# Performance work log

Measured on AMD Instinct MI355X. Metric: run time of the kernel, lower is better.

Reference implementation:

```python
import jax, jax.numpy as jnp
import numpy as np

HIDDEN = 1024
NUM_HEAD = 16
HEAD_DIM = HIDDEN // NUM_HEAD


def setup_inputs() -> dict:
    key = jax.random.key(0)
    ks = jax.random.split(key, 9)
    B, S = 1, 4096
    scale = 1.0 / np.sqrt(HIDDEN)
    inp = {
        "x": jax.random.normal(ks[0], (B, S, HIDDEN), dtype=jnp.float32),
        "wq": jax.random.normal(ks[1], (HIDDEN, HIDDEN), dtype=jnp.float32) * scale,
        "bq": jnp.zeros((HIDDEN,), dtype=jnp.float32),
        "wk": jax.random.normal(ks[2], (HIDDEN, HIDDEN), dtype=jnp.float32) * scale,
        "bk": jnp.zeros((HIDDEN,), dtype=jnp.float32),
        "wv": jax.random.normal(ks[3], (HIDDEN, HIDDEN), dtype=jnp.float32) * scale,
        "bv": jnp.zeros((HIDDEN,), dtype=jnp.float32),
        "wo": jax.random.normal(ks[4], (HIDDEN, HIDDEN), dtype=jnp.float32) * scale,
        "bo": jnp.zeros((HIDDEN,), dtype=jnp.float32),
    }
    return inp


def reference(x, wq, bq, wk, bk, wv, bv, wo, bo):
    B, S, _ = x.shape
    # QKV projections (torch Linear: x @ W.T + b)
    def split_heads(t):
        return t.reshape(B, S, NUM_HEAD, HEAD_DIM).transpose(0, 2, 1, 3)  # [B,H,S,D]
    q = split_heads(x @ wq.T + bq)
    k = split_heads(x @ wk.T + bk)
    v = split_heads(x @ wv.T + bv)
    # scaled dot-product scores: [B,H,S,S]
    scores = jnp.einsum('bhsd,bhtd->bhst', q, k) / jnp.sqrt(jnp.float32(HEAD_DIM))
    # faithful double softmax over the key axis (no mask; dropout = eval identity)
    attn = jax.nn.softmax(scores, axis=-1)
    attn = jax.nn.softmax(attn, axis=-1)
    out = jnp.einsum('bhst,bhtd->bhsd', attn, v)  # [B,H,S,D]
    out = out.transpose(0, 2, 1, 3).reshape(B, S, HIDDEN)
    return out @ wo.T + bo
```

## Files before the change

### kernel.cpp

```cpp
#include <hip/hip_runtime.h>
#include <hip/hip_bf16.h>
#include <stdint.h>

#define S 4096
#define HID 1024
#define NH 16
#define DH 64

typedef __attribute__((ext_vector_type(8))) short short8;
typedef __attribute__((ext_vector_type(2))) float f32x2;
typedef __attribute__((ext_vector_type(4))) float f32x4;
typedef __attribute__((ext_vector_type(16))) float f32x16;
typedef __attribute__((ext_vector_type(4))) unsigned int u32x4;

#define VMCNT8 asm volatile("s_waitcnt vmcnt(8)" ::: "memory")
#define VMCNT0 asm volatile("s_waitcnt vmcnt(0)" ::: "memory")
#define LGKM0  asm volatile("s_waitcnt lgkmcnt(0)" ::: "memory")

__device__ __forceinline__ unsigned short f2bf(float f) {
  unsigned int u = __builtin_bit_cast(unsigned int, f);
  u += 0x7FFF + ((u >> 16) & 1);
  return (unsigned short)(u >> 16);
}
__device__ __forceinline__ unsigned int pktrunc(float lo, float hi) {
  return __builtin_amdgcn_perm(__builtin_bit_cast(unsigned int, hi),
                               __builtin_bit_cast(unsigned int, lo), 0x07060302u);
}
__device__ __forceinline__ void gload16(const unsigned short* g, unsigned short* l) {
  __builtin_amdgcn_global_load_lds((const __attribute__((address_space(1))) unsigned int*)g,
                                   (__attribute__((address_space(3))) unsigned int*)l, 16, 0, 0);
}

__global__ __launch_bounds__(256) void cast_kernel(
    const float* __restrict__ x,  const float* __restrict__ wq,
    const float* __restrict__ wk, const float* __restrict__ wv,
    const float* __restrict__ wo,
    unsigned short* __restrict__ xb,  unsigned short* __restrict__ wqb,
    unsigned short* __restrict__ wkb, unsigned short* __restrict__ wvb,
    unsigned short* __restrict__ wob, float* __restrict__ vsum)
{
  int y = blockIdx.y;
  const float* src; unsigned short* dst; int n;
  if      (y == 0) { src = x;  dst = xb;  n = S * HID; }
  else if (y == 1) { src = wq; dst = wqb; n = HID * HID; }
  else if (y == 2) { src = wk; dst = wkb; n = HID * HID; }
  else if (y == 3) { src = wv; dst = wvb; n = HID * HID; }
  else             { src = wo; dst = wob; n = HID * HID; }
  if (y == 0 && blockIdx.x == 0) {
    f32x4 z = {0.f, 0.f, 0.f, 0.f};
    reinterpret_cast<f32x4*>(vsum)[threadIdx.x] = z;
  }
  int i = (blockIdx.x * 256 + threadIdx.x) * 4;
  if (i < n) {
    float4 v = *reinterpret_cast<const float4*>(src + i);
    ushort4 o;
    o.x = f2bf(v.x); o.y = f2bf(v.y); o.z = f2bf(v.z); o.w = f2bf(v.w);
    *reinterpret_cast<ushort4*>(dst + i) = o;
  }
}

__device__ __forceinline__ void gemm128(
    const unsigned short* __restrict__ A, const unsigned short* __restrict__ W,
    unsigned short* As, unsigned short* Bs, f32x4 acc[4][4], int row0, int col0)
{
  const int tid = threadIdx.x;
  const int wave = tid >> 6, lane = tid & 63, quad = lane >> 4, l16 = lane & 15;
  const int wr = (wave >> 1) * 64, wc = (wave & 1) * 64;
  const int srow = lane >> 2, sseg = lane & 3;
  const f32x4 z = {0.f, 0.f, 0.f, 0.f};
  #pragma unroll
  for (int i = 0; i < 4; i++)
    #pragma unroll
    for (int j = 0; j < 4; j++) acc[i][j] = z;

  for (int k0 = 0; k0 < HID; k0 += 32) {
    __syncthreads();
    #pragma unroll
    for (int c = 0; c < 2; c++) {
      const int rbase = c * 64 + wave * 16;
      gload16(A + (size_t)(row0 + rbase + srow) * HID + k0 + sseg * 8, As + rbase * 32);
      gload16(W + (size_t)(col0 + rbase + srow) * HID + k0 + sseg * 8, Bs + rbase * 32);
    }
    __syncthreads();

    short8 af[4], bfr[4];
    #pragma unroll
    for (int i = 0; i < 4; i++)
      af[i] = *reinterpret_cast<const short8*>(As + (wr + i * 16 + l16) * 32 + quad * 8);
    #pragma unroll
    for (int j = 0; j < 4; j++)
      bfr[j] = *reinterpret_cast<const short8*>(Bs + (wc + j * 16 + l16) * 32 + quad * 8);
    #pragma unroll
    for (int i = 0; i < 4; i++)
      #pragma unroll
      for (int j = 0; j < 4; j++)
        acc[i][j] = __builtin_amdgcn_mfma_f32_16x16x32_bf16(af[i], bfr[j], acc[i][j], 0, 0, 0);
  }
}

__global__ __launch_bounds__(256) void qkv_gemm_kernel(
    const unsigned short* __restrict__ X,
    const unsigned short* __restrict__ Wq, const unsigned short* __restrict__ Wk,
    const unsigned short* __restrict__ Wv,
    const float* __restrict__ bq, const float* __restrict__ bk, const float* __restrict__ bv,
    unsigned short* __restrict__ Qo, unsigned short* __restrict__ K2o, unsigned short* __restrict__ Vbo,
    float* __restrict__ Vsum)
{
  __shared__ unsigned short As[128 * 32];
  __shared__ unsigned short Bs[128 * 32];
  __shared__ unsigned short Ep[16384];
  const int zsel = blockIdx.z;
  const unsigned short* W = (zsel == 0) ? Wq : (zsel == 1) ? Wk : Wv;
  const float* bias        = (zsel == 0) ? bq : (zsel == 1) ? bk : bv;
  const int row0 = blockIdx.x * 128, col0 = blockIdx.y * 128;
  f32x4 acc[4][4];
  gemm128(X, W, As, Bs, acc, row0, col0);

  const int tid = threadIdx.x;
  const int wave = tid >> 6, lane = tid & 63, quad = lane >> 4, l16 = lane & 15;
  const int wr = (wave >> 1) * 64, wc = (wave & 1) * 64;
  const int h0 = col0 >> 6, g0 = row0 >> 5;

  if (zsel == 0) {
    const float osc = 0.18033688011112042f;
    #pragma unroll
    for (int j = 0; j < 4; j++) {
      int rc = wc + j * 16 + l16;
      float bb = bias[col0 + rc];
      int hh = rc >> 6, d = rc & 63;
      #pragma unroll
      for (int i = 0; i < 4; i++)
        #pragma unroll
        for (int rr = 0; rr < 4; rr++) {
          int srel = wr + i * 16 + quad * 4 + rr;
          Ep[hh * 8192 + srel * 64 + d] = f2bf((acc[i][j][rr] + bb) * osc);
        }
    }
  } else if (zsel == 1) {
    #pragma unroll
    for (int j = 0; j < 4; j++) {
      int rc = wc + j * 16 + l16;
      float bb = bias[col0 + rc];
      int hh = rc >> 6, dh = rc & 63;
      int c = dh >> 4, hfk = (dh >> 3) & 1, j8 = dh & 7;
      #pragma unroll
      for (int i = 0; i < 4; i++)
        #pragma unroll
        for (int rr = 0; rr < 4; rr++) {
          int srel = wr + i * 16 + quad * 4 + rr;
          int gl = srel >> 5, l32k = srel & 31;
          Ep[(hh * 4 + gl) * 2048 + (c * 64 + hfk * 32 + l32k) * 8 + j8] =
              f2bf(acc[i][j][rr] + bb);
        }
    }
  } else {
    #pragma unroll
    for (int j = 0; j < 4; j++) {
      int rc = wc + j * 16 + l16;
      float bb = bias[col0 + rc];
      int hh = rc >> 6, dh = rc & 63;
      int ng = dh >> 5, l32v = dh & 31;
      int hf_v = quad & 1, jj0 = (quad >> 1) * 4;
      float colsum = 0.f;
      #pragma unroll
      for (int i = 0; i < 4; i++) {
        int gt4 = (wr + i * 16) >> 5;
        int grp = i & 1;
        float v0 = acc[i][j][0] + bb, v1 = acc[i][j][1] + bb;
        float v2 = acc[i][j][2] + bb, v3 = acc[i][j][3] + bb;
        colsum += (v0 + v1) + (v2 + v3);
        ushort4 pv;
        pv.x = f2bf(v0); pv.y = f2bf(v1); pv.z = f2bf(v2); pv.w = f2bf(v3);
        *reinterpret_cast<ushort4*>(
            Ep + (((hh * 4 + gt4) * 2 + grp) * 2 + ng) * 512 + (hf_v * 32 + l32v) * 8 + jj0) = pv;
      }
      colsum += __shfl_xor(colsum, 16);
      colsum += __shfl_xor(colsum, 32);
      if (quad == 0) atomicAdd(&Vsum[col0 + rc], colsum);
    }
  }
  __syncthreads();

  #pragma unroll
  for (int it = 0; it < 8; it++) {
    int flat = it * 2048 + tid * 8;
    u32x4 v = *reinterpret_cast<const u32x4*>(Ep + flat);
    if (zsel == 0) {
      int hh = flat >> 13;
      size_t goff = ((size_t)(h0 + hh) * S + row0) * 64 + (flat & 8191);
      *reinterpret_cast<u32x4*>(Qo + goff) = v;
    } else if (zsel == 1) {
      int sp = flat >> 11, hh = sp >> 2, g4 = sp & 3;
      size_t goff = (size_t)((h0 + hh) * 128 + g0 + g4) * 2048 + (flat & 2047);
      *reinterpret_cast<u32x4*>(K2o + goff) = v;
    } else {
      int sp = flat >> 9;
      int ng = sp & 1, grp = (sp >> 1) & 1, gt4 = (sp >> 2) & 3, hh = sp >> 4;
      size_t goff = (size_t)((((h0 + hh) * 128 + g0 + gt4) * 2 + grp) * 2 + ng) * 512 + (flat & 511);
      *reinterpret_cast<u32x4*>(Vbo + goff) = v;
    }
  }
}

__global__ __launch_bounds__(256) void out_gemm_kernel(
    const unsigned short* __restrict__ A, const unsigned short* __restrict__ W,
    const float* __restrict__ be, float* __restrict__ dst)
{
  __shared__ unsigned short As[128 * 32];
  __shared__ unsigned short Bs[128 * 32];
  const int row0 = blockIdx.x * 128, col0 = blockIdx.y * 128;
  f32x4 acc[4][4];
  gemm128(A, W, As, Bs, acc, row0, col0);

  const int tid = threadIdx.x;
  const int wave = tid >> 6, lane = tid & 63, quad = lane >> 4, l16 = lane & 15;
  const int wr = (wave >> 1) * 64, wc = (wave & 1) * 64;
  #pragma unroll
  for (int j = 0; j < 4; j++) {
    int n = col0 + wc + j * 16 + l16;
    float bb = be[n];
    #pragma unroll
    for (int i = 0; i < 4; i++)
      #pragma unroll
      for (int rr = 0; rr < 4; rr++) {
        int s = row0 + wr + i * 16 + quad * 4 + rr;
        dst[(size_t)s * HID + n] = acc[i][j][rr] + bb;
      }
  }
}

__global__ __launch_bounds__(256) void biasfold_kernel(
    const float* __restrict__ Vsum, const float* __restrict__ wo,
    const float* __restrict__ bo, float* __restrict__ be)
{
  const int n = blockIdx.x * 4 + (threadIdx.x >> 6);
  const int l = threadIdx.x & 63;
  float acc = 0.f;
  #pragma unroll
  for (int i = 0; i < 16; i++)
    acc += Vsum[l + 64 * i] * wo[(size_t)n * HID + l + 64 * i];
  #pragma unroll
  for (int off = 32; off >= 1; off >>= 1) acc += __shfl_xor(acc, off);
  if (l == 0) be[n] = bo[n] + acc * (1.f / 4097.f);
}

struct AttnState {
  short8 qf[2][4];
  f32x16 Oa[2][2];
  f32x16 zacc;
  f32x2  zp[2];
};

__device__ __forceinline__ void loadregs(
    const unsigned short* kb, const unsigned short* vb,
    short8 (&kf)[4], short8 (&vf)[4])
{
  #pragma unroll
  for (int c = 0; c < 4; c++)
    kf[c] = *reinterpret_cast<const short8*>(kb + c * 512);
  #pragma unroll
  for (int w = 0; w < 4; w++)
    vf[w] = *reinterpret_cast<const short8*>(vb + w * 512);
}

__device__ __forceinline__ void attn_compute(
    const short8 (&kf)[4], const short8 (&vfr)[4], AttnState& st)
{
  #pragma unroll
  for (int qh = 0; qh < 2; qh++) {
    f32x16 acc = __builtin_amdgcn_mfma_f32_32x32x16_bf16(kf[0], st.qf[qh][0], st.zacc, 0, 0, 0);
    #pragma unroll
    for (int c = 1; c < 4; c++)
      acc = __builtin_amdgcn_mfma_f32_32x32x16_bf16(kf[c], st.qf[qh][c], acc, 0, 0, 0);

    unsigned int D[8];
    #pragma unroll
    for (int m = 0; m < 8; m++) {
      float t0 = __builtin_amdgcn_exp2f(acc[2 * m]);
      float t1 = __builtin_amdgcn_exp2f(acc[2 * m + 1]);
      f32x2 t = {t0, t1};
      st.zp[qh] += t;
      D[m] = pktrunc(t0, t1);
    }
    u32x4 dv0 = {D[0], D[1], D[2], D[3]};
    u32x4 dv1 = {D[4], D[5], D[6], D[7]};
    short8 A0 = __builtin_bit_cast(short8, dv0);
    short8 A1 = __builtin_bit_cast(short8, dv1);

    st.Oa[qh][0] = __builtin_amdgcn_mfma_f32_32x32x16_bf16(A0, vfr[0], st.Oa[qh][0], 0, 0, 0);
    st.Oa[qh][1] = __builtin_amdgcn_mfma_f32_32x32x16_bf16(A0, vfr[1], st.Oa[qh][1], 0, 0, 0);
    st.Oa[qh][0] = __builtin_amdgcn_mfma_f32_32x32x16_bf16(A1, vfr[2], st.Oa[qh][0], 0, 0, 0);
    st.Oa[qh][1] = __builtin_amdgcn_mfma_f32_32x32x16_bf16(A1, vfr[3], st.Oa[qh][1], 0, 0, 0);
  }
}

__device__ __forceinline__ void stage_tile(
    const unsigned short* gK, const unsigned short* gV,
    unsigned short* lK, unsigned short* lV)
{
  #pragma unroll
  for (int i = 0; i < 4; i++) gload16(gK + i * 512, lK + i * 512);
  #pragma unroll
  for (int i = 0; i < 4; i++) gload16(gV + i * 512, lV + i * 512);
}

__global__ __launch_bounds__(256, 2) void attn_kernel(
    const unsigned short* __restrict__ Q, const unsigned short* __restrict__ K2,
    const unsigned short* __restrict__ Vb, unsigned short* __restrict__ OUT)
{
  __shared__ unsigned short T[4][2][2][2048];
  __shared__ float Zl[256];
  float* Ored = reinterpret_cast<float*>(&T[0][0][0][0]);

  const int lin = blockIdx.y * 64 + blockIdx.x;
  const int xcd = lin & 7, idx = lin >> 3;
  const int h = xcd * 2 + (idx >> 6);
  const int q0 = (idx & 63) * 64;

  const int tid = threadIdx.x;
  const int wave = tid >> 6, lane = tid & 63, hf = lane >> 5, l32 = lane & 31;

  AttnState st;
  #pragma unroll
  for (int qh = 0; qh < 2; qh++) {
    const unsigned short* qrow = Q + (size_t)(h * S + q0 + qh * 32 + l32) * DH;
    #pragma unroll
    for (int c = 0; c < 4; c++)
      st.qf[qh][c] = *reinterpret_cast<const short8*>(qrow + c * 16 + hf * 8);
  }
  #pragma unroll
  for (int r = 0; r < 16; r++) {
    st.zacc[r] = 0.f;
    st.Oa[0][0][r] = 0.f; st.Oa[0][1][r] = 0.f;
    st.Oa[1][0][r] = 0.f; st.Oa[1][1][r] = 0.f;
  }
  st.zp[0] = (f32x2){0.f, 0.f};
  st.zp[1] = (f32x2){0.f, 0.f};

  const unsigned short* Kb  = K2 + (size_t)h * 128 * 2048;
  const unsigned short* Vbb = Vb + (size_t)h * 128 * 2048;

  const unsigned short* gK = Kb  + (size_t)wave * 2048 + (size_t)lane * 8;
  const unsigned short* gV = Vbb + (size_t)wave * 2048 + (size_t)lane * 8;
  unsigned short* lK0 = &T[wave][0][0][0];
  unsigned short* lV0 = &T[wave][0][1][0];
  unsigned short* lK1 = &T[wave][1][0][0];
  unsigned short* lV1 = &T[wave][1][1][0];
  const unsigned short* kb0 = &T[wave][0][0][0] + lane * 8;
  const unsigned short* vb0 = &T[wave][0][1][0] + lane * 8;
  const unsigned short* kb1 = &T[wave][1][0][0] + lane * 8;
  const unsigned short* vb1 = &T[wave][1][1][0] + lane * 8;
  const ptrdiff_t STR = 4 * 2048;

  short8 kA[4], vA[4], kB[4], vB[4];

  stage_tile(gK, gV, lK0, lV0); gK += STR; gV += STR;
  VMCNT0;
  loadregs(kb0, vb0, kA, vA);
  stage_tile(gK, gV, lK1, lV1); gK += STR; gV += STR;
  LGKM0;

  for (int p = 0; p < 15; p++) {
    stage_tile(gK, gV, lK0, lV0); gK += STR; gV += STR;
    VMCNT8;
    loadregs(kb1, vb1, kB, vB);
    attn_compute(kA, vA, st);
    LGKM0;
    stage_tile(gK, gV, lK1, lV1); gK += STR; gV += STR;
    VMCNT8;
    loadregs(kb0, vb0, kA, vA);
    attn_compute(kB, vB, st);
    LGKM0;
  }
  VMCNT0;
  loadregs(kb1, vb1, kB, vB);
  attn_compute(kA, vA, st);
  attn_compute(kB, vB, st);

  __syncthreads();
  {
    float za = st.zp[0][0] + st.zp[0][1];
    float zb = st.zp[1][0] + st.zp[1][1];
    za += __shfl_xor(za, 32);
    zb += __shfl_xor(zb, 32);
    if (hf == 0) {
      Zl[wave * 64 + l32]      = za;
      Zl[wave * 64 + 32 + l32] = zb;
    }
    float* Ow = Ored + wave * 4096;
    #pragma unroll
    for (int qh = 0; qh < 2; qh++)
      #pragma unroll
      for (int ng = 0; ng < 2; ng++)
        #pragma unroll
        for (int r = 0; r < 16; r++) {
          const int row = (r & 3) + 8 * (r >> 2) + 4 * hf;
          Ow[(qh * 32 + row) * 64 + ng * 32 + l32] = st.Oa[qh][ng][r];
        }
  }
  __syncthreads();
  {
    const int q = tid >> 2, d0 = (tid & 3) * 16;
    const float* O0 = Ored + q * 64 + d0;
    f32x4 s0 = *reinterpret_cast<const f32x4*>(O0);
    f32x4 s1 = *reinterpret_cast<const f32x4*>(O0 + 4);
    f32x4 s2 = *reinterpret_cast<const f32x4*>(O0 + 8);
    f32x4 s3 = *reinterpret_cast<const f32x4*>(O0 + 12);
    #pragma unroll
    for (int w = 1; w < 4; w++) {
      const float* Ow = Ored + w * 4096 + q * 64 + d0;
      s0 += *reinterpret_cast<const f32x4*>(Ow);
      s1 += *reinterpret_cast<const f32x4*>(Ow + 4);
      s2 += *reinterpret_cast<const f32x4*>(Ow + 8);
      s3 += *reinterpret_cast<const f32x4*>(Ow + 12);
    }
    const float zt = Zl[q] + Zl[64 + q] + Zl[128 + q] + Zl[192 + q];
    const float rz = 1.f / (zt * 4097.f);
    unsigned short* op = OUT + (size_t)(q0 + q) * HID + h * DH + d0;
    ushort4 u;
    u.x = f2bf(s0[0] * rz); u.y = f2bf(s0[1] * rz);
    u.z = f2bf(s0[2] * rz); u.w = f2bf(s0[3] * rz);
    *reinterpret_cast<ushort4*>(op) = u;
    u.x = f2bf(s1[0] * rz); u.y = f2bf(s1[1] * rz);
    u.z = f2bf(s1[2] * rz); u.w = f2bf(s1[3] * rz);
    *reinterpret_cast<ushort4*>(op + 4) = u;
    u.x = f2bf(s2[0] * rz); u.y = f2bf(s2[1] * rz);
    u.z = f2bf(s2[2] * rz); u.w = f2bf(s2[3] * rz);
    *reinterpret_cast<ushort4*>(op + 8) = u;
    u.x = f2bf(s3[0] * rz); u.y = f2bf(s3[1] * rz);
    u.z = f2bf(s3[2] * rz); u.w = f2bf(s3[3] * rz);
    *reinterpret_cast<ushort4*>(op + 12) = u;
  }
}

extern "C" void kernel_launch(void* const* d_in, const int* in_sizes, int n_in,
                              void* d_out, int out_size, void* d_ws, size_t ws_size,
                              hipStream_t stream) {
  const float* x  = (const float*)d_in[0];
  const float* wq = (const float*)d_in[1];
  const float* bq = (const float*)d_in[2];
  const float* wk = (const float*)d_in[3];
  const float* bk = (const float*)d_in[4];
  const float* wv = (const float*)d_in[5];
  const float* bv = (const float*)d_in[6];
  const float* wo = (const float*)d_in[7];
  const float* bo = (const float*)d_in[8];
  float* out = (float*)d_out;

  char* ws = (char*)d_ws;
  unsigned short* xb  = (unsigned short*)(ws);
  unsigned short* wqb = (unsigned short*)(ws + (8u  << 20));
  unsigned short* wkb = (unsigned short*)(ws + (10u << 20));
  unsigned short* wvb = (unsigned short*)(ws + (12u << 20));
  unsigned short* wob = (unsigned short*)(ws + (14u << 20));
  unsigned short* qw  = (unsigned short*)(ws + (16u << 20));
  unsigned short* k2  = (unsigned short*)(ws + (24u << 20));
  unsigned short* vb  = (unsigned short*)(ws + (32u << 20));
  float* vsum         = (float*)(ws + (40u << 20));
  float* be           = (float*)(ws + (40u << 20) + 65536);
  unsigned short* aw  = xb;

  cast_kernel<<<dim3(4096, 5), 256, 0, stream>>>(x, wq, wk, wv, wo, xb, wqb, wkb, wvb, wob, vsum);
  qkv_gemm_kernel<<<dim3(32, 8, 3), 256, 0, stream>>>(xb, wqb, wkb, wvb, bq, bk, bv, qw, k2, vb, vsum);
  biasfold_kernel<<<dim3(256), 256, 0, stream>>>(vsum, wo, bo, be);
  attn_kernel<<<dim3(64, 16), 256, 0, stream>>>(qw, k2, vb, aw);
  out_gemm_kernel<<<dim3(32, 8, 1), 256, 0, stream>>>(aw, wob, be, out);
}
```

Before: 234.3 us.

## Fold bias-fold kernel into attention launch, compact cast grid, add MFMA priority

The separate biasfold kernel becomes an extra row of blocks (blockIdx.y==16) in the attention launch, which removes one kernel launch and its serialization. The cast kernel's grid is reshaped to 1024x8 with no idle blocks and no bounds check. s_setprio hints are placed around the MFMA sequences in the attention inner loop to favor matrix issue. The extra attention blocks finish quickly but take scheduling slots. Because the bias blocks sit at the end of the grid, the XCD mapping of the attention blocks is unchanged.

```diff
diff --git a/kernel.cpp b/kernel.cpp
--- a/kernel.cpp
+++ b/kernel.cpp
@@ -39,24 +39,22 @@
     unsigned short* __restrict__ wkb, unsigned short* __restrict__ wvb,
     unsigned short* __restrict__ wob, float* __restrict__ vsum)
 {
-  int y = blockIdx.y;
-  const float* src; unsigned short* dst; int n;
-  if      (y == 0) { src = x;  dst = xb;  n = S * HID; }
-  else if (y == 1) { src = wq; dst = wqb; n = HID * HID; }
-  else if (y == 2) { src = wk; dst = wkb; n = HID * HID; }
-  else if (y == 3) { src = wv; dst = wvb; n = HID * HID; }
-  else             { src = wo; dst = wob; n = HID * HID; }
-  if (y == 0 && blockIdx.x == 0) {
+  const int y = blockIdx.y, bx = blockIdx.x;
+  const float* src; unsigned short* dst; int cx;
+  if (y < 4)       { src = x;  dst = xb;  cx = y * 1024 + bx; }
+  else if (y == 4) { src = wq; dst = wqb; cx = bx; }
+  else if (y == 5) { src = wk; dst = wkb; cx = bx; }
+  else if (y == 6) { src = wv; dst = wvb; cx = bx; }
+  else             { src = wo; dst = wob; cx = bx; }
+  if (y == 4 && bx == 0) {
     f32x4 z = {0.f, 0.f, 0.f, 0.f};
     reinterpret_cast<f32x4*>(vsum)[threadIdx.x] = z;
   }
-  int i = (blockIdx.x * 256 + threadIdx.x) * 4;
-  if (i < n) {
-    float4 v = *reinterpret_cast<const float4*>(src + i);
-    ushort4 o;
-    o.x = f2bf(v.x); o.y = f2bf(v.y); o.z = f2bf(v.z); o.w = f2bf(v.w);
-    *reinterpret_cast<ushort4*>(dst + i) = o;
-  }
+  int i = (cx * 256 + threadIdx.x) * 4;
+  float4 v = *reinterpret_cast<const float4*>(src + i);
+  ushort4 o;
+  o.x = f2bf(v.x); o.y = f2bf(v.y); o.z = f2bf(v.z); o.w = f2bf(v.w);
+  *reinterpret_cast<ushort4*>(dst + i) = o;
 }
 
 __device__ __forceinline__ void gemm128(
@@ -229,21 +227,6 @@
   }
 }
 
-__global__ __launch_bounds__(256) void biasfold_kernel(
-    const float* __restrict__ Vsum, const float* __restrict__ wo,
-    const float* __restrict__ bo, float* __restrict__ be)
-{
-  const int n = blockIdx.x * 4 + (threadIdx.x >> 6);
-  const int l = threadIdx.x & 63;
-  float acc = 0.f;
-  #pragma unroll
-  for (int i = 0; i < 16; i++)
-    acc += Vsum[l + 64 * i] * wo[(size_t)n * HID + l + 64 * i];
-  #pragma unroll
-  for (int off = 32; off >= 1; off >>= 1) acc += __shfl_xor(acc, off);
-  if (l == 0) be[n] = bo[n] + acc * (1.f / 4097.f);
-}
-
 struct AttnState {
   short8 qf[2][4];
   f32x16 Oa[2][2];
@@ -268,10 +251,12 @@
 {
   #pragma unroll
   for (int qh = 0; qh < 2; qh++) {
+    __builtin_amdgcn_s_setprio(1);
     f32x16 acc = __builtin_amdgcn_mfma_f32_32x32x16_bf16(kf[0], st.qf[qh][0], st.zacc, 0, 0, 0);
     #pragma unroll
     for (int c = 1; c < 4; c++)
       acc = __builtin_amdgcn_mfma_f32_32x32x16_bf16(kf[c], st.qf[qh][c], acc, 0, 0, 0);
+    __builtin_amdgcn_s_setprio(0);
 
     unsigned int D[8];
     #pragma unroll
@@ -287,10 +272,12 @@
     short8 A0 = __builtin_bit_cast(short8, dv0);
     short8 A1 = __builtin_bit_cast(short8, dv1);
 
+    __builtin_amdgcn_s_setprio(1);
     st.Oa[qh][0] = __builtin_amdgcn_mfma_f32_32x32x16_bf16(A0, vfr[0], st.Oa[qh][0], 0, 0, 0);
     st.Oa[qh][1] = __builtin_amdgcn_mfma_f32_32x32x16_bf16(A0, vfr[1], st.Oa[qh][1], 0, 0, 0);
     st.Oa[qh][0] = __builtin_amdgcn_mfma_f32_32x32x16_bf16(A1, vfr[2], st.Oa[qh][0], 0, 0, 0);
     st.Oa[qh][1] = __builtin_amdgcn_mfma_f32_32x32x16_bf16(A1, vfr[3], st.Oa[qh][1], 0, 0, 0);
+    __builtin_amdgcn_s_setprio(0);
   }
 }
 
@@ -306,8 +293,27 @@
 
 __global__ __launch_bounds__(256, 2) void attn_kernel(
     const unsigned short* __restrict__ Q, const unsigned short* __restrict__ K2,
-    const unsigned short* __restrict__ Vb, unsigned short* __restrict__ OUT)
-{
+    const unsigned short* __restrict__ Vb, unsigned short* __restrict__ OUT,
+    const float* __restrict__ Vsum, const float* __restrict__ wo,
+    const float* __restrict__ bo, float* __restrict__ be)
+{
+  if (blockIdx.y == 16) {
+    const int base = blockIdx.x * 16 + (threadIdx.x >> 6) * 4;
+    const int l = threadIdx.x & 63;
+    #pragma unroll
+    for (int c = 0; c < 4; c++) {
+      const int n = base + c;
+      float acc = 0.f;
+      #pragma unroll
+      for (int i = 0; i < 16; i++)
+        acc += Vsum[l + 64 * i] * wo[(size_t)n * HID + l + 64 * i];
+      #pragma unroll
+      for (int off = 32; off >= 1; off >>= 1) acc += __shfl_xor(acc, off);
+      if (l == 0) be[n] = bo[n] + acc * (1.f / 4097.f);
+    }
+    return;
+  }
+
   __shared__ unsigned short T[4][2][2][2048];
   __shared__ float Zl[256];
   float* Ored = reinterpret_cast<float*>(&T[0][0][0][0]);
@@ -460,9 +466,8 @@
   float* be           = (float*)(ws + (40u << 20) + 65536);
   unsigned short* aw  = xb;
 
-  cast_kernel<<<dim3(4096, 5), 256, 0, stream>>>(x, wq, wk, wv, wo, xb, wqb, wkb, wvb, wob, vsum);
+  cast_kernel<<<dim3(1024, 8), 256, 0, stream>>>(x, wq, wk, wv, wo, xb, wqb, wkb, wvb, wob, vsum);
   qkv_gemm_kernel<<<dim3(32, 8, 3), 256, 0, stream>>>(xb, wqb, wkb, wvb, bq, bk, bv, qw, k2, vb, vsum);
-  biasfold_kernel<<<dim3(256), 256, 0, stream>>>(vsum, wo, bo, be);
-  attn_kernel<<<dim3(64, 16), 256, 0, stream>>>(qw, k2, vb, aw);
+  attn_kernel<<<dim3(64, 17), 256, 0, stream>>>(qw, k2, vb, aw, vsum, wo, bo, be);
   out_gemm_kernel<<<dim3(32, 8, 1), 256, 0, stream>>>(aw, wob, be, out);
 }
```

New measurement: 236.9 us. No clear change (+1.1%).
